# Optimization experiments

Measured on AMD Instinct MI355X. Metric: run time of the kernel, lower is better.

## Reference

```python
import jax, jax.numpy as jnp
import numpy as np

ALPHA, BETA, GAMMA = 1.0, 0.01, 0.1
COS_EPS = 1e-8  # torch F.cosine_similarity eps


def setup_inputs() -> dict:
    key = jax.random.key(0)
    k1, k2, k3, k4 = jax.random.split(key, 4)
    B, C = 4096, 1000
    N, D = 8192, 256
    return {
        "pred": jax.random.normal(k1, (B, C), dtype=jnp.float32),
        "target": jax.random.randint(k2, (B,), 0, C, dtype=jnp.int64),
        "adj_matrix": jax.random.uniform(k3, (N, N), dtype=jnp.float32),
        "node_embeddings": jax.random.normal(k4, (N, D), dtype=jnp.float32),
    }


def reference(pred, target, adj_matrix, node_embeddings):
    # L_task: mean cross-entropy over logits
    logp = jax.nn.log_softmax(pred, axis=-1)                      # [B, C]
    l_task = -jnp.mean(jnp.take_along_axis(logp, target[:, None], axis=1))

    # L_sparse: mean |adj|
    l_sparse = jnp.mean(jnp.abs(adj_matrix))

    # L_semantic: cosine similarity via normalize + matmul (avoids NxNxD intermediate)
    norms = jnp.linalg.norm(node_embeddings, axis=1)              # [N]
    dots = node_embeddings @ node_embeddings.T                    # [N, N]
    sim = dots / jnp.maximum(norms[:, None] * norms[None, :], COS_EPS)
    l_semantic = jnp.mean(adj_matrix * (1.0 - sim))

    return ALPHA * l_task + BETA * l_sparse + GAMMA * l_semantic
```

## Files before the change

kernel.cpp:

```cpp
#include <hip/hip_runtime.h>
#include <hip/hip_bf16.h>
#include <stdint.h>
#include <stddef.h>

#define N_NODES 8192
#define DIM     256
#define BATCH   4096
#define CLASSES 1000
#define ALPHA_C 1.0f
#define BETA_C  0.01f
#define GAMMA_C 0.1f

typedef __bf16 bf16_t;
typedef __bf16 bf16x8 __attribute__((ext_vector_type(8)));
typedef __bf16 bf16x4 __attribute__((ext_vector_type(4)));
typedef float  f32x4  __attribute__((ext_vector_type(4)));
typedef float  f32x16 __attribute__((ext_vector_type(16)));

__device__ __forceinline__ void async16(const void* g, void* l) {
  __builtin_amdgcn_global_load_lds(
      (const __attribute__((address_space(1))) uint32_t*)g,
      (__attribute__((address_space(3))) uint32_t*)l, 16, 0, 0);
}

__global__ __launch_bounds__(256) void prep_kernel(
    const float* __restrict__ emb, bf16_t* __restrict__ U) {
  const int row = blockIdx.x;
  const int t = threadIdx.x;
  const float v = emb[(size_t)row * DIM + t];
  float sq = v * v;
  for (int off = 32; off; off >>= 1) sq += __shfl_down(sq, off);
  __shared__ float red[4];
  if ((t & 63) == 0) red[t >> 6] = sq;
  __syncthreads();
  const float total = red[0] + red[1] + red[2] + red[3];
  U[(size_t)row * DIM + t] = (bf16_t)(v * rsqrtf(total));
}

__global__ __launch_bounds__(256) void transpose_kernel(
    const bf16_t* __restrict__ U, bf16_t* __restrict__ Ut) {
  __shared__ bf16_t tile[64][72];
  const int i0 = blockIdx.x * 64, d0 = blockIdx.y * 64;
  const int t = threadIdx.x;
  const int r = t >> 3, c8 = (t & 7) * 8;
#pragma unroll
  for (int it = 0; it < 2; ++it) {
    const int row = r + it * 32;
    *(bf16x8*)&tile[row][c8] =
        *(const bf16x8*)&U[(size_t)(i0 + row) * DIM + d0 + c8];
  }
  __syncthreads();
#pragma unroll
  for (int it = 0; it < 2; ++it) {
    const int d = r + it * 32;
    bf16x8 v;
#pragma unroll
    for (int j = 0; j < 8; ++j) v[j] = tile[c8 + j][d];
    *(bf16x8*)&Ut[(size_t)(d0 + d) * N_NODES + i0 + c8] = v;
  }
}

__global__ __launch_bounds__(256) void ce_kernel(
    const float* __restrict__ pred, const int* __restrict__ target,
    float* __restrict__ out) {
  const int row = blockIdx.x;
  const int t = threadIdx.x;
  const float* p = pred + (size_t)row * CLASSES;

  float v[4];
  for (int k = 0; k < 4; ++k) {
    const int c = t + k * 256;
    v[k] = (c < CLASSES) ? p[c] : -INFINITY;
  }

  float m = fmaxf(fmaxf(v[0], v[1]), fmaxf(v[2], v[3]));
  for (int off = 32; off; off >>= 1) m = fmaxf(m, __shfl_down(m, off));

  __shared__ float red[8];
  const int wave = t >> 6, lane = t & 63;
  if (lane == 0) red[wave] = m;
  __syncthreads();
  if (t == 0) red[4] = fmaxf(fmaxf(red[0], red[1]), fmaxf(red[2], red[3]));
  __syncthreads();
  const float mx = red[4];

  float s = 0.f;
  for (int k = 0; k < 4; ++k) s += __expf(v[k] - mx);
  for (int off = 32; off; off >>= 1) s += __shfl_down(s, off);
  if (lane == 0) red[wave] = s;
  __syncthreads();
  if (t == 0) {
    float ssum = red[0] + red[1] + red[2] + red[3];
    float lse = mx + __logf(ssum);
    float loss = lse - p[target[row]];
    atomicAdd(out, loss * (ALPHA_C / (float)BATCH));
  }
}

#define BN 128
#define KW 256
#define KC (N_NODES / KW)
#define NKS (KW / 16)
#define PF 8

__global__ __launch_bounds__(512, 2) void semantic_kernel(
    const float* __restrict__ adj, const bf16_t* __restrict__ U,
    const bf16_t* __restrict__ Ut, float* __restrict__ out) {
  __shared__ __align__(16) bf16_t lds_ut[DIM * KW];
  __shared__ float red[8];

  const int t = threadIdx.x;
  const int w = t >> 6, lane = t & 63;
  const int wm = w >> 2, wn = w & 3;
  const int m = lane & 31, h = lane >> 5;
  const int i0 = blockIdx.x * BN;
  const int k0 = blockIdx.y * KW;

  f32x16 acc[4] = {};
  float s_abs = 0.f, s_sum = 0.f;

  const float* ap = adj + (size_t)(i0 + wn * 32 + m) * N_NODES + k0 + h * 8;

  f32x4 pb[PF][2];
#pragma unroll
  for (int ks = 0; ks < PF; ++ks) {
    pb[ks][0] = *(const f32x4*)(ap + ks * 16);
    pb[ks][1] = *(const f32x4*)(ap + ks * 16 + 4);
  }

  {
    const int rl = lane >> 5;
    const int p = lane & 31;
#pragma unroll
    for (int ii = 0; ii < 16; ++ii) {
      const int rbase = w * 32 + ii * 2;
      const int r = rbase + rl;
      async16(Ut + (size_t)r * N_NODES + k0 + ((p ^ (r & 31)) * 8),
              &lds_ut[rbase * KW]);
    }
  }
  __syncthreads();

#pragma unroll
  for (int ks = 0; ks < NKS; ++ks) {
    const int s = ks & (PF - 1);
    const f32x4 b0 = pb[s][0];
    const f32x4 b1 = pb[s][1];
    if (ks + PF < NKS) {
      pb[s][0] = *(const f32x4*)(ap + (ks + PF) * 16);
      pb[s][1] = *(const f32x4*)(ap + (ks + PF) * 16 + 4);
    }

    bf16x8 af[4];
#pragma unroll
    for (int mr = 0; mr < 4; ++mr) {
      const int rd = wm * 128 + mr * 32 + m;
      af[mr] = *(const bf16x8*)&lds_ut[rd * KW + (((ks * 2 + h) ^ m) * 8)];
    }

    if (wm == 0) {
      s_abs += fabsf(b0[0]) + fabsf(b0[1]) + fabsf(b0[2]) + fabsf(b0[3]) +
               fabsf(b1[0]) + fabsf(b1[1]) + fabsf(b1[2]) + fabsf(b1[3]);
      s_sum += b0[0] + b0[1] + b0[2] + b0[3] + b1[0] + b1[1] + b1[2] + b1[3];
    }

    bf16x8 bb;
    bb[0] = (bf16_t)b0[0]; bb[1] = (bf16_t)b0[1];
    bb[2] = (bf16_t)b0[2]; bb[3] = (bf16_t)b0[3];
    bb[4] = (bf16_t)b1[0]; bb[5] = (bf16_t)b1[1];
    bb[6] = (bf16_t)b1[2]; bb[7] = (bf16_t)b1[3];
#pragma unroll
    for (int mr = 0; mr < 4; ++mr)
      acc[mr] = __builtin_amdgcn_mfma_f32_32x32x16_bf16(af[mr], bb, acc[mr],
                                                        0, 0, 0);
  }

  float tr = 0.f;
  const bf16_t* Urow = U + (size_t)(i0 + wn * 32 + m) * DIM;
#pragma unroll
  for (int mr = 0; mr < 4; ++mr) {
#pragma unroll
    for (int rq = 0; rq < 4; ++rq) {
      const int d = wm * 128 + mr * 32 + rq * 8 + h * 4;
      const bf16x4 uu = *(const bf16x4*)&Urow[d];
      tr += acc[mr][rq * 4 + 0] * (float)uu[0] +
            acc[mr][rq * 4 + 1] * (float)uu[1] +
            acc[mr][rq * 4 + 2] * (float)uu[2] +
            acc[mr][rq * 4 + 3] * (float)uu[3];
    }
  }

  float contrib = -GAMMA_C * tr;
  if (wm == 0) contrib += BETA_C * s_abs + GAMMA_C * s_sum;
  for (int off = 32; off; off >>= 1) contrib += __shfl_down(contrib, off);
  if (lane == 0) red[w] = contrib;
  __syncthreads();
  if (t == 0) {
    float tot = 0.f;
    for (int i = 0; i < 8; ++i) tot += red[i];
    const float inv = 1.f / ((float)N_NODES * (float)N_NODES);
    atomicAdd(out, tot * inv);
  }
}

extern "C" void kernel_launch(void* const* d_in, const int* in_sizes, int n_in,
                              void* d_out, int out_size, void* d_ws,
                              size_t ws_size, hipStream_t stream) {
  const float* pred   = (const float*)d_in[0];
  const int*   target = (const int*)d_in[1];
  const float* adj    = (const float*)d_in[2];
  const float* emb    = (const float*)d_in[3];
  float* out = (float*)d_out;

  bf16_t* U  = (bf16_t*)d_ws;
  bf16_t* Ut = U + (size_t)N_NODES * DIM;

  hipMemsetAsync(d_out, 0, sizeof(float), stream);
  prep_kernel<<<N_NODES, 256, 0, stream>>>(emb, U);
  transpose_kernel<<<dim3(N_NODES / 64, DIM / 64), 256, 0, stream>>>(U, Ut);
  ce_kernel<<<BATCH, 256, 0, stream>>>(pred, target, out);
  semantic_kernel<<<dim3(N_NODES / BN, KC), 512, 0, stream>>>(adj, U, Ut, out);
}
```

Baseline: 485.3 us.

## Stage adj and Ut tiles through LDS with register prefetch over longer K ranges

The semantic kernel now processes 2048-wide K ranges per block in 128-wide chunks instead of 256-wide ranges. Both adj (converted to bf16) and Ut are staged through padded LDS tiles, and the next chunk is prefetched into registers while the current one feeds the MFMAs. adj is now read from global memory once per element with coalesced row loads, rather than being streamed directly into registers by two wave groups. The cost is two barriers per chunk, a single LDS buffer, and a grid of only 256 blocks, which may leave the GPU under-occupied.

New measurement: 445.0 us. -8.3%, faster.

```diff
diff --git a/kernel.cpp b/kernel.cpp
--- a/kernel.cpp
+++ b/kernel.cpp
@@ -17,12 +17,6 @@
 typedef float  f32x4  __attribute__((ext_vector_type(4)));
 typedef float  f32x16 __attribute__((ext_vector_type(16)));
 
-__device__ __forceinline__ void async16(const void* g, void* l) {
-  __builtin_amdgcn_global_load_lds(
-      (const __attribute__((address_space(1))) uint32_t*)g,
-      (__attribute__((address_space(3))) uint32_t*)l, 16, 0, 0);
-}
-
 __global__ __launch_bounds__(256) void prep_kernel(
     const float* __restrict__ emb, bf16_t* __restrict__ U) {
   const int row = blockIdx.x;
@@ -98,15 +92,16 @@
 }
 
 #define BN 128
-#define KW 256
-#define KC (N_NODES / KW)
-#define NKS (KW / 16)
-#define PF 8
+#define BK 128
+#define KW 2048
+#define NCH (KW / BK)
+#define SP  (BK + 8)
 
 __global__ __launch_bounds__(512, 2) void semantic_kernel(
     const float* __restrict__ adj, const bf16_t* __restrict__ U,
     const bf16_t* __restrict__ Ut, float* __restrict__ out) {
-  __shared__ __align__(16) bf16_t lds_ut[DIM * KW];
+  __shared__ __align__(16) bf16_t a_lds[BN * SP];
+  __shared__ __align__(16) bf16_t ut_lds[DIM * SP];
   __shared__ float red[8];
 
   const int t = threadIdx.x;
@@ -119,60 +114,65 @@
   f32x16 acc[4] = {};
   float s_abs = 0.f, s_sum = 0.f;
 
-  const float* ap = adj + (size_t)(i0 + wn * 32 + m) * N_NODES + k0 + h * 8;
-
-  f32x4 pb[PF][2];
-#pragma unroll
-  for (int ks = 0; ks < PF; ++ks) {
-    pb[ks][0] = *(const f32x4*)(ap + ks * 16);
-    pb[ks][1] = *(const f32x4*)(ap + ks * 16 + 4);
-  }
-
-  {
-    const int rl = lane >> 5;
-    const int p = lane & 31;
-#pragma unroll
-    for (int ii = 0; ii < 16; ++ii) {
-      const int rbase = w * 32 + ii * 2;
-      const int r = rbase + rl;
-      async16(Ut + (size_t)r * N_NODES + k0 + ((p ^ (r & 31)) * 8),
-              &lds_ut[rbase * KW]);
+  const int arow0 = w * 16 + (lane >> 5);
+  const int acol = (lane & 31) * 4;
+  const int urow0 = w * 32 + (lane >> 4);
+  const int ucol = (lane & 15) * 8;
+
+  f32x4 adjs[8];
+  bf16x8 uts[8];
+
+  auto LOADC = [&](int c) {
+    const size_t kb = (size_t)k0 + (size_t)c * BK;
+#pragma unroll
+    for (int j = 0; j < 8; ++j)
+      adjs[j] = *(const f32x4*)
+          &adj[(size_t)(i0 + arow0 + j * 2) * N_NODES + kb + acol];
+#pragma unroll
+    for (int j = 0; j < 8; ++j)
+      uts[j] = *(const bf16x8*)
+          &Ut[(size_t)(urow0 + j * 4) * N_NODES + kb + ucol];
+  };
+
+  auto WRITEC = [&]() {
+#pragma unroll
+    for (int j = 0; j < 8; ++j) {
+      const f32x4 v = adjs[j];
+      s_abs += fabsf(v[0]) + fabsf(v[1]) + fabsf(v[2]) + fabsf(v[3]);
+      s_sum += v[0] + v[1] + v[2] + v[3];
+      bf16x4 b;
+      b[0] = (bf16_t)v[0]; b[1] = (bf16_t)v[1];
+      b[2] = (bf16_t)v[2]; b[3] = (bf16_t)v[3];
+      *(bf16x4*)&a_lds[(arow0 + j * 2) * SP + acol] = b;
     }
-  }
-  __syncthreads();
-
-#pragma unroll
-  for (int ks = 0; ks < NKS; ++ks) {
-    const int s = ks & (PF - 1);
-    const f32x4 b0 = pb[s][0];
-    const f32x4 b1 = pb[s][1];
-    if (ks + PF < NKS) {
-      pb[s][0] = *(const f32x4*)(ap + (ks + PF) * 16);
-      pb[s][1] = *(const f32x4*)(ap + (ks + PF) * 16 + 4);
+#pragma unroll
+    for (int j = 0; j < 8; ++j)
+      *(bf16x8*)&ut_lds[(urow0 + j * 4) * SP + ucol] = uts[j];
+  };
+
+  LOADC(0);
+  WRITEC();
+  __syncthreads();
+
+  for (int c = 0; c < NCH; ++c) {
+    if (c + 1 < NCH) LOADC(c + 1);
+#pragma unroll
+    for (int ks = 0; ks < 8; ++ks) {
+      bf16x8 af[4];
+#pragma unroll
+      for (int mr = 0; mr < 4; ++mr)
+        af[mr] = *(const bf16x8*)
+            &ut_lds[(wm * 128 + mr * 32 + m) * SP + ks * 16 + h * 8];
+      const bf16x8 bfr = *(const bf16x8*)
+          &a_lds[(wn * 32 + m) * SP + ks * 16 + h * 8];
+#pragma unroll
+      for (int mr = 0; mr < 4; ++mr)
+        acc[mr] = __builtin_amdgcn_mfma_f32_32x32x16_bf16(af[mr], bfr,
+                                                          acc[mr], 0, 0, 0);
     }
-
-    bf16x8 af[4];
-#pragma unroll
-    for (int mr = 0; mr < 4; ++mr) {
-      const int rd = wm * 128 + mr * 32 + m;
-      af[mr] = *(const bf16x8*)&lds_ut[rd * KW + (((ks * 2 + h) ^ m) * 8)];
-    }
-
-    if (wm == 0) {
-      s_abs += fabsf(b0[0]) + fabsf(b0[1]) + fabsf(b0[2]) + fabsf(b0[3]) +
-               fabsf(b1[0]) + fabsf(b1[1]) + fabsf(b1[2]) + fabsf(b1[3]);
-      s_sum += b0[0] + b0[1] + b0[2] + b0[3] + b1[0] + b1[1] + b1[2] + b1[3];
-    }
-
-    bf16x8 bb;
-    bb[0] = (bf16_t)b0[0]; bb[1] = (bf16_t)b0[1];
-    bb[2] = (bf16_t)b0[2]; bb[3] = (bf16_t)b0[3];
-    bb[4] = (bf16_t)b1[0]; bb[5] = (bf16_t)b1[1];
-    bb[6] = (bf16_t)b1[2]; bb[7] = (bf16_t)b1[3];
-#pragma unroll
-    for (int mr = 0; mr < 4; ++mr)
-      acc[mr] = __builtin_amdgcn_mfma_f32_32x32x16_bf16(af[mr], bb, acc[mr],
-                                                        0, 0, 0);
+    __syncthreads();
+    if (c + 1 < NCH) WRITEC();
+    __syncthreads();
   }
 
   float tr = 0.f;
@@ -190,8 +190,7 @@
     }
   }
 
-  float contrib = -GAMMA_C * tr;
-  if (wm == 0) contrib += BETA_C * s_abs + GAMMA_C * s_sum;
+  float contrib = BETA_C * s_abs + GAMMA_C * s_sum - GAMMA_C * tr;
   for (int off = 32; off; off >>= 1) contrib += __shfl_down(contrib, off);
   if (lane == 0) red[w] = contrib;
   __syncthreads();
@@ -219,5 +218,6 @@
   prep_kernel<<<N_NODES, 256, 0, stream>>>(emb, U);
   transpose_kernel<<<dim3(N_NODES / 64, DIM / 64), 256, 0, stream>>>(U, Ut);
   ce_kernel<<<BATCH, 256, 0, stream>>>(pred, target, out);
-  semantic_kernel<<<dim3(N_NODES / BN, KC), 512, 0, stream>>>(adj, U, Ut, out);
-}
+  semantic_kernel<<<dim3(N_NODES / BN, KW == N_NODES ? 1 : N_NODES / KW), 512,
+                    0, stream>>>(adj, U, Ut, out);
+}
```
